# Optimization experiments

Measured on AMD Instinct MI355X. Metric: run time of the kernel, lower is better.

## Reference

```python
import jax, jax.numpy as jnp
import numpy as np

D = 128          # model_dim
R = 4            # num_relations
H = 64           # hidden width from num_neurons=[64, 64]
N = 50000        # num nodes
E = 800000       # num edges (avg degree 16)
NUM_NODE_TYPES = 3
UPDATE_NODE_TYPES = (0, 1)  # static update_node_type_indices
# update_edge_type_indices = range(R) (all relations), closed over statically


def setup_inputs() -> dict:
    key = jax.random.key(0)
    ks = jax.random.split(key, 12)
    s = 0.05
    return dict(
        node_feature=jax.random.normal(ks[0], (N, D), jnp.float32),
        src=jax.random.randint(ks[1], (E,), 0, N, dtype=jnp.int32),
        dst=jax.random.randint(ks[2], (E,), 0, N, dtype=jnp.int32),
        edge_type=jax.random.randint(ks[3], (E,), 0, R, dtype=jnp.int32),
        node_type=jax.random.randint(ks[4], (N,), 0, NUM_NODE_TYPES, dtype=jnp.int32),
        # per-relation MLP params, stacked over relations
        W1=jax.random.normal(ks[5], (R, D, H), jnp.float32) * s,
        b1=jnp.zeros((R, H), jnp.float32),
        W2=jax.random.normal(ks[6], (R, H, H), jnp.float32) * s,
        b2=jnp.zeros((R, H), jnp.float32),
        W3=jax.random.normal(ks[7], (R, H, D), jnp.float32) * s,
        b3=jnp.zeros((R, D), jnp.float32),
        # node updater: (R+1)*D -> H -> H -> D
        Wu1=jax.random.normal(ks[8], (D * (R + 1), H), jnp.float32) * s,
        bu1=jnp.zeros((H,), jnp.float32),
        Wu2=jax.random.normal(ks[9], (H, H), jnp.float32) * s,
        bu2=jnp.zeros((H,), jnp.float32),
        Wu3=jax.random.normal(ks[10], (H, D), jnp.float32) * s,
        bu3=jnp.zeros((D,), jnp.float32),
    )


def _mlp(x, W1, b1, W2, b2, W3, b3):
    # MLP with ReLU hidden layers, linear output (torch MLP(in, out, [64,64]))
    h = jax.nn.relu(x @ W1 + b1)
    h = jax.nn.relu(h @ W2 + b2)
    return h @ W3 + b3


def reference(node_feature, src, dst, edge_type, node_type,
              W1, b1, W2, b2, W3, b3, Wu1, bu1, Wu2, bu2, Wu3, bu3):
    n = node_feature.shape[0]
    sf = node_feature[src]  # [E, D] gather source features once

    # DGL send_and_recv only writes aggregated features to nodes that receive
    # at least one message; others are zero-filled. Track in-degree > 0.
    indeg = jax.ops.segment_sum(jnp.ones(dst.shape, node_feature.dtype), dst,
                                num_segments=n)
    has_in = (indeg > 0).astype(node_feature.dtype)[:, None]

    blocks = [jax.nn.relu(node_feature) * has_in]  # first D-block of enc input
    for i in range(W1.shape[0]):  # static loop over relations
        msg = jax.nn.relu(_mlp(sf, W1[i], b1[i], W2[i], b2[i], W3[i], b3[i]))
        msg = msg * (edge_type == i)[:, None]  # zero msg for other relations
        blocks.append(jax.ops.segment_sum(msg, dst, num_segments=n))
    enc = jnp.concatenate(blocks, axis=-1)  # [N, (R+1)*D]

    upd = _mlp(enc, Wu1, bu1, Wu2, bu2, Wu3, bu3)  # [N, D]
    upd_mask = jnp.zeros(node_type.shape, bool)
    for t in UPDATE_NODE_TYPES:
        upd_mask = upd_mask | (node_type == t)
    return jnp.where(upd_mask[:, None], upd, node_feature)
```

## Files before the change

### kernel.cpp

```cpp
#include <hip/hip_runtime.h>
#include <hip/hip_bf16.h>

#define D 128
#define H 64
#define R 4
#define NT 64
#define LDC 132
#define CAP 64
#define CCAP 4608
#define EPB 2048

typedef __attribute__((ext_vector_type(8))) short bf16x8;
typedef __attribute__((ext_vector_type(4))) float f32x4;

#define PREL 56
#define PFRAG 512
#define UBASE (R * PREL)
#define UPREL 40
#define NFRAG (UBASE + UPREL)

__device__ __forceinline__ float4 relu4(float4 v) {
    return make_float4(fmaxf(v.x, 0.f), fmaxf(v.y, 0.f), fmaxf(v.z, 0.f), fmaxf(v.w, 0.f));
}

__device__ __forceinline__ unsigned short f2bf_rne(float x) {
    unsigned u = __float_as_uint(x);
    return (unsigned short)((u + 0x7fffu + ((u >> 16) & 1u)) >> 16);
}

__device__ __forceinline__ void split1(float x, short& hi, short& lo) {
    unsigned u = __float_as_uint(x);
    unsigned hb = u & 0xffff0000u;
    float res = x - __uint_as_float(hb);
    hi = (short)(u >> 16);
    lo = (short)(__float_as_uint(res) >> 16);
}

__device__ __forceinline__ void split8(const float* x8, bf16x8& hi, bf16x8& lo) {
#pragma unroll
    for (int i = 0; i < 8; ++i) {
        short h, l;
        split1(x8[i], h, l);
        hi[i] = h; lo[i] = l;
    }
}

__device__ __forceinline__ void load_split_A(const float* ap, bf16x8& ah, bf16x8& al) {
    float x8[8];
    *(float4*)&x8[0] = *(const float4*)ap;
    *(float4*)&x8[4] = *(const float4*)(ap + 4);
    split8(x8, ah, al);
}

template<int KSTEPS>
__device__ __forceinline__ void split_strip_A(const float* Ws, int lane, bf16x8* ah, bf16x8* al) {
#pragma unroll
    for (int ks = 0; ks < KSTEPS; ++ks)
        load_split_A(Ws + (lane & 15) * LDC + ks * 32 + ((lane >> 4) << 3), ah[ks], al[ks]);
}

__device__ __forceinline__ void gload_lds16(const void* g, void* l) {
    __builtin_amdgcn_global_load_lds(
        (const __attribute__((address_space(1))) void*)g,
        (__attribute__((address_space(3))) void*)l, 16, 0, 0);
}

__device__ __forceinline__ void stage_chunk(const short* __restrict__ srcH,
                                            short* BbH, int w, int lane) {
#pragma unroll
    for (int f = w; f < 8; f += 4)
        gload_lds16(srcH + ((size_t)f << 9) + (lane << 3), BbH + (f << 9));
}

template<int NCH, int KSTEPS>
__device__ __forceinline__ void compute_chunk(const bf16x8* ah, const bf16x8* al,
                                              const short* BbH,
                                              const short* __restrict__ BloG,
                                              int lane, f32x4* acc) {
#pragma unroll
    for (int ks = 0; ks < KSTEPS; ++ks) {
        bf16x8 bh[NCH], bl[NCH];
#pragma unroll
        for (int n = 0; n < NCH; ++n) {
            int f = n * KSTEPS + ks;
            bh[n] = *(const bf16x8*)(BbH + ((f * 64 + lane) << 3));
            bl[n] = *(const bf16x8*)(BloG + (((size_t)f * 64 + lane) << 3));
        }
#pragma unroll
        for (int n = 0; n < NCH; ++n) {
            acc[n] = __builtin_amdgcn_mfma_f32_16x16x32_bf16(ah[ks], bh[n], acc[n], 0, 0, 0);
            acc[n] = __builtin_amdgcn_mfma_f32_16x16x32_bf16(ah[ks], bl[n], acc[n], 0, 0, 0);
            acc[n] = __builtin_amdgcn_mfma_f32_16x16x32_bf16(al[ks], bh[n], acc[n], 0, 0, 0);
        }
    }
}

template<int NT_TILES, int KSTEPS>
__device__ __forceinline__ void mfma_layer(const float* Als, int ld,
                                           const short* __restrict__ Bhi,
                                           const short* __restrict__ Blo,
                                           int lane, f32x4* acc) {
#pragma unroll
    for (int ks = 0; ks < KSTEPS; ++ks) {
        bf16x8 ah, al;
        load_split_A(Als + (lane & 15) * ld + ks * 32 + ((lane >> 4) << 3), ah, al);
        bf16x8 bh[NT_TILES], bl[NT_TILES];
#pragma unroll
        for (int n = 0; n < NT_TILES; ++n) {
            int f = n * KSTEPS + ks;
            bh[n] = *(const bf16x8*)(Bhi + (((size_t)f * 64 + lane) << 3));
            bl[n] = *(const bf16x8*)(Blo + (((size_t)f * 64 + lane) << 3));
        }
#pragma unroll
        for (int n = 0; n < NT_TILES; ++n) {
            acc[n] = __builtin_amdgcn_mfma_f32_16x16x32_bf16(ah, bh[n], acc[n], 0, 0, 0);
            acc[n] = __builtin_amdgcn_mfma_f32_16x16x32_bf16(ah, bl[n], acc[n], 0, 0, 0);
            acc[n] = __builtin_amdgcn_mfma_f32_16x16x32_bf16(al, bh[n], acc[n], 0, 0, 0);
        }
    }
}

template<int NT_TILES, int KSTEPS>
__device__ __forceinline__ void mfma_layer_regA(const bf16x8* ah, const bf16x8* al,
                                                const short* __restrict__ Bhi,
                                                const short* __restrict__ Blo,
                                                int lane, f32x4* acc) {
#pragma unroll
    for (int ks = 0; ks < KSTEPS; ++ks) {
        bf16x8 bh[NT_TILES], bl[NT_TILES];
#pragma unroll
        for (int n = 0; n < NT_TILES; ++n) {
            int f = n * KSTEPS + ks;
            bh[n] = *(const bf16x8*)(Bhi + (((size_t)f * 64 + lane) << 3));
            bl[n] = *(const bf16x8*)(Blo + (((size_t)f * 64 + lane) << 3));
        }
#pragma unroll
        for (int n = 0; n < NT_TILES; ++n) {
            acc[n] = __builtin_amdgcn_mfma_f32_16x16x32_bf16(ah[ks], bh[n], acc[n], 0, 0, 0);
            acc[n] = __builtin_amdgcn_mfma_f32_16x16x32_bf16(ah[ks], bl[n], acc[n], 0, 0, 0);
            acc[n] = __builtin_amdgcn_mfma_f32_16x16x32_bf16(al[ks], bh[n], acc[n], 0, 0, 0);
        }
    }
}

template<int NT_TILES>
__device__ __forceinline__ void store_C_lds(const f32x4* acc, const float* __restrict__ bias,
                                            float* Ld, int ld, int lane) {
    int r0 = (lane >> 4) << 2;
#pragma unroll
    for (int n = 0; n < NT_TILES; ++n) {
        int col = n * 16 + (lane & 15);
        float bv = bias[col];
#pragma unroll
        for (int q = 0; q < 4; ++q)
            Ld[(r0 + q) * ld + col] = fmaxf(acc[n][q] + bv, 0.f);
    }
}


__global__ __launch_bounds__(256) void k_prep(
    const float* __restrict__ W1, const float* __restrict__ W2,
    const float* __restrict__ W3, const float* __restrict__ Wu1,
    const float* __restrict__ Wu2, const float* __restrict__ Wu3,
    short* __restrict__ Phi, short* __restrict__ Plo,
    const int* __restrict__ esrc, const int* __restrict__ dst,
    const int* __restrict__ etype, int* __restrict__ gcnt,
    int2* __restrict__ coarse, int E, int NB)
{
    __shared__ int hist[256];
    __shared__ int base[256];
    const int t = threadIdx.x;

    if (blockIdx.x < 19) {
        int pair = blockIdx.x;
        const float* src; int KS, NTl, fragbase, ncol;
        if (pair < 16) {
            int r = pair >> 2, mat = pair & 3;
            if (mat == 0)      { src = W1  + (size_t)r * (D * H);       KS = 4; NTl = 4; fragbase = r * PREL + 0;  ncol = 64;  }
            else if (mat == 1) { src = W2  + (size_t)r * (H * H);       KS = 2; NTl = 4; fragbase = r * PREL + 16; ncol = 64;  }
            else if (mat == 2) { src = W3  + (size_t)r * (H * D);       KS = 2; NTl = 8; fragbase = r * PREL + 24; ncol = 128; }
            else               { src = Wu1 + (size_t)(r + 1) * D * H;   KS = 4; NTl = 4; fragbase = r * PREL + 40; ncol = 64;  }
        } else {
            int mat = pair - 16;
            if (mat == 0)      { src = Wu1; KS = 4; NTl = 4; fragbase = UBASE + 0;  ncol = 64;  }
            else if (mat == 1) { src = Wu2; KS = 2; NTl = 4; fragbase = UBASE + 16; ncol = 64;  }
            else               { src = Wu3; KS = 2; NTl = 8; fragbase = UBASE + 24; ncol = 128; }
        }
        int nf = NTl * KS;
        for (int u = t; u < nf * 64; u += 256) {
            int f = u >> 6, lane = u & 63;
            int n = f / KS, ks = f - n * KS;
            int col = n * 16 + (lane & 15);
            int k0 = ks * 32 + ((lane >> 4) << 3);
            size_t dstp = (((size_t)(fragbase + f)) * 64 + (size_t)lane) * 8;
#pragma unroll
            for (int i = 0; i < 8; ++i) {
                short h, l;
                split1(src[(size_t)(k0 + i) * ncol + col], h, l);
                Phi[dstp + i] = h;
                Plo[dstp + i] = l;
            }
        }
        return;
    }

    const int e0 = (blockIdx.x - 19) * EPB;
    hist[t] = 0;
    __syncthreads();
    int dsav[8], rsav[8];
#pragma unroll
    for (int j = 0; j < 8; ++j) {
        int e = e0 + j * 256 + t;
        int d = -1, rk = 0;
        if (e < E) {
            d = dst[e];
            rk = atomicAdd(&hist[d >> 8], 1);
        }
        dsav[j] = d; rsav[j] = rk;
    }
    __syncthreads();
    if (t < NB) base[t] = atomicAdd(&gcnt[t], hist[t]);
    __syncthreads();
#pragma unroll
    for (int j = 0; j < 8; ++j) {
        int e = e0 + j * 256 + t;
        int d = dsav[j];
        if (d >= 0) {
            int bin = d >> 8;
            int pos = base[bin] + rsav[j];
            if (pos < CCAP)
                coarse[(size_t)bin * CCAP + pos] = make_int2(d, esrc[e] * 4 + etype[e]);
        }
    }
}


__global__ __launch_bounds__(256, 3) void k_mlp_bin(
    const float* __restrict__ X,
    const float* __restrict__ b1, const float* __restrict__ b2, const float* __restrict__ b3,
    const short* __restrict__ Phi, const short* __restrict__ Plo,
    unsigned short* __restrict__ U, int N, int tiles,
    const int2* __restrict__ coarse, const int* __restrict__ gcnt,
    int* __restrict__ cnt, int* __restrict__ eidx, int NB)
{
    __shared__ float Bsh[NT * LDC];
    __shared__ short BbH[2][8 * PFRAG];

    const int tid = threadIdx.x;
    const int bid = blockIdx.x;

    if (bid < NB) {
        int* lcnt = (int*)Bsh;
        lcnt[tid] = 0;
        __syncthreads();
        int m = gcnt[bid]; if (m > CCAP) m = CCAP;
        const int2* cp = coarse + (size_t)bid * CCAP;
        for (int i = tid; i < m; i += 256) {
            int2 pr = cp[i];
            int p = atomicAdd(&lcnt[pr.x & 255], 1);
            if (p < CAP) eidx[(size_t)pr.x * CAP + p] = pr.y;
        }
        __syncthreads();
        int node = (bid << 8) + tid;
        if (node < N) cnt[node] = lcnt[tid];
        return;
    }

    const int mi = bid - NB;
    const int lane = tid & 63;
    const int w = tid >> 6;
    const int m16 = w * 16;
    const int r = mi / tiles;
    const int n0 = (mi - r * tiles) * NT;

    const short* PH = Phi + (size_t)(r * PREL) * PFRAG;
    const short* PL = Plo + (size_t)(r * PREL) * PFRAG;
    const float* b1r = b1 + r * H;
    const float* b2r = b2 + r * H;
    const float* b3r = b3 + r * D;

    float* Ws = &Bsh[m16 * LDC];

    stage_chunk(PH,             BbH[0], w, lane);
    stage_chunk(PH + 8 * PFRAG, BbH[1], w, lane);

    bf16x8 ahx[4], alx[4];
    {
        int row = n0 + m16 + (lane & 15);
        const float* xp = X + (size_t)row * D + ((lane >> 4) << 3);
        bool ok = (row < N);
#pragma unroll
        for (int ks = 0; ks < 4; ++ks) {
            float x8[8];
            if (ok) {
                *(float4*)&x8[0] = *(const float4*)(xp + ks * 32);
                *(float4*)&x8[4] = *(const float4*)(xp + ks * 32 + 4);
            } else {
#pragma unroll
                for (int i = 0; i < 8; ++i) x8[i] = 0.f;
            }
            split8(x8, ahx[ks], alx[ks]);
        }
    }
    __syncthreads();

    f32x4 acc[8];
#pragma unroll
    for (int n = 0; n < 4; ++n) acc[n] = (f32x4){0.f, 0.f, 0.f, 0.f};
    compute_chunk<2, 4>(ahx, alx, BbH[0], PL, lane, acc + 0);
    __syncthreads();
    stage_chunk(PH + 16 * PFRAG, BbH[0], w, lane);
    compute_chunk<2, 4>(ahx, alx, BbH[1], PL + 8 * PFRAG, lane, acc + 2);
    store_C_lds<4>(acc, b1r, Ws, LDC, lane);
    __syncthreads();
    stage_chunk(PH + 24 * PFRAG, BbH[1], w, lane);

    bf16x8 a2h[2], a2l[2];
    split_strip_A<2>(Ws, lane, a2h, a2l);
#pragma unroll
    for (int n = 0; n < 4; ++n) acc[n] = (f32x4){0.f, 0.f, 0.f, 0.f};
    compute_chunk<4, 2>(a2h, a2l, BbH[0], PL + 16 * PFRAG, lane, acc);
    store_C_lds<4>(acc, b2r, Ws, LDC, lane);
    __syncthreads();
    stage_chunk(PH + 32 * PFRAG, BbH[0], w, lane);

    bf16x8 a3h[2], a3l[2];
    split_strip_A<2>(Ws, lane, a3h, a3l);
#pragma unroll
    for (int n = 0; n < 8; ++n) acc[n] = (f32x4){0.f, 0.f, 0.f, 0.f};
    compute_chunk<4, 2>(a3h, a3l, BbH[1], PL + 24 * PFRAG, lane, acc + 0);
    __syncthreads();
    stage_chunk(PH + 40 * PFRAG, BbH[1], w, lane);
    compute_chunk<4, 2>(a3h, a3l, BbH[0], PL + 32 * PFRAG, lane, acc + 4);
    store_C_lds<8>(acc, b3r, Ws, LDC, lane);
    __syncthreads();
    stage_chunk(PH + 48 * PFRAG, BbH[0], w, lane);

    bf16x8 auh[4], aul[4];
    split_strip_A<4>(Ws, lane, auh, aul);
    f32x4 accu[4];
#pragma unroll
    for (int n = 0; n < 4; ++n) accu[n] = (f32x4){0.f, 0.f, 0.f, 0.f};
    compute_chunk<2, 4>(auh, aul, BbH[1], PL + 40 * PFRAG, lane, accu + 0);
    __syncthreads();
    compute_chunk<2, 4>(auh, aul, BbH[0], PL + 48 * PFRAG, lane, accu + 2);
    {
        int r0 = (lane >> 4) << 2;
#pragma unroll
        for (int n = 0; n < 4; ++n) {
            int col = n * 16 + (lane & 15);
#pragma unroll
            for (int q = 0; q < 4; ++q) {
                int node = n0 + m16 + r0 + q;
                if (node < N)
                    U[((size_t)node * R + r) * H + col] = f2bf_rne(accu[n][q]);
            }
        }
    }
}


__global__ __launch_bounds__(256) void k_gather(
    const unsigned int* __restrict__ U32,
    const int* __restrict__ cnt, const int* __restrict__ eidx,
    float* __restrict__ S, int N)
{
    const int wid = threadIdx.x >> 6, lane = threadIdx.x & 63;
    const int n = blockIdx.x * 4 + wid;
    if (n >= N) return;
    int g = cnt[n]; if (g > CAP) g = CAP;
    const int* ep = eidx + (size_t)n * CAP;
    const int half = lane >> 5;
    const int c2 = lane & 31;
    float ax = 0.f, ay = 0.f;
    {
        int m = g;
        int v = 0;
        if (lane < m) v = ep[lane];
        for (int j0 = 0; j0 < m; j0 += 16) {
            int lim = m - j0; if (lim > 16) lim = 16;
            unsigned t[8];
#pragma unroll
            for (int p = 0; p < 8; ++p) {
                int vi = __shfl(v, j0 + 2 * p + half);
                bool ok = (2 * p + half) < lim;
                t[p] = ok ? U32[(size_t)vi * 32 + c2] : 0u;
            }
#pragma unroll
            for (int p = 0; p < 8; ++p) {
                ax += __uint_as_float(t[p] << 16);
                ay += __uint_as_float(t[p] & 0xffff0000u);
            }
        }
    }
    ax += __shfl_xor(ax, 32);
    ay += __shfl_xor(ay, 32);
    if (half == 0)
        *(float2*)&S[(size_t)n * H + (c2 << 1)] = make_float2(ax, ay);
}


__global__ __launch_bounds__(256, 4) void k_upd(
    const float* __restrict__ X, const float* __restrict__ S,
    const int* __restrict__ cnt, const int* __restrict__ node_type,
    const short* __restrict__ Phi, const short* __restrict__ Plo,
    const float* __restrict__ bu1, const float* __restrict__ bu2, const float* __restrict__ bu3,
    float* __restrict__ out, int N)
{
    __shared__ float Hsh[NT * LDC];

    const int tid = threadIdx.x;
    const int lane = tid & 63;
    const int w = tid >> 6;
    const int m16 = w * 16;
    const int n0 = blockIdx.x * NT;

    const short* PH = Phi + (size_t)UBASE * PFRAG;
    const short* PL = Plo + (size_t)UBASE * PFRAG;

    float* Ws = &Hsh[m16 * LDC];

    bf16x8 ahx[4], alx[4];
    {
        int row = n0 + m16 + (lane & 15);
        bool ok = (row < N) && (cnt[row] > 0);
        const float* xp = X + (size_t)row * D + ((lane >> 4) << 3);
#pragma unroll
        for (int ks = 0; ks < 4; ++ks) {
            float x8[8];
            if (ok) {
                float4 a = *(const float4*)(xp + ks * 32);
                float4 b = *(const float4*)(xp + ks * 32 + 4);
                a = relu4(a); b = relu4(b);
                *(float4*)&x8[0] = a;
                *(float4*)&x8[4] = b;
            } else {
#pragma unroll
                for (int i = 0; i < 8; ++i) x8[i] = 0.f;
            }
            split8(x8, ahx[ks], alx[ks]);
        }
    }

    f32x4 acc[8];
#pragma unroll
    for (int n = 0; n < 4; ++n) acc[n] = (f32x4){0.f, 0.f, 0.f, 0.f};
    mfma_layer_regA<4, 4>(ahx, alx, PH, PL, lane, acc);
    {
        int r0 = (lane >> 4) << 2;
#pragma unroll
        for (int n = 0; n < 4; ++n) {
            int col = n * 16 + (lane & 15);
            float bv = bu1[col];
#pragma unroll
            for (int q = 0; q < 4; ++q) {
                int node = n0 + m16 + r0 + q;
                float sv = (node < N) ? S[(size_t)node * H + col] : 0.f;
                Ws[(r0 + q) * LDC + col] = fmaxf(acc[n][q] + bv + sv, 0.f);
            }
        }
    }

#pragma unroll
    for (int n = 0; n < 4; ++n) acc[n] = (f32x4){0.f, 0.f, 0.f, 0.f};
    mfma_layer<4, 2>(Ws, LDC, PH + (size_t)16 * PFRAG, PL + (size_t)16 * PFRAG, lane, acc);
    store_C_lds<4>(acc, bu2, Ws, LDC, lane);

#pragma unroll
    for (int n = 0; n < 8; ++n) acc[n] = (f32x4){0.f, 0.f, 0.f, 0.f};
    mfma_layer<8, 2>(Ws, LDC, PH + (size_t)24 * PFRAG, PL + (size_t)24 * PFRAG, lane, acc);
    {
        int r0 = (lane >> 4) << 2;
#pragma unroll
        for (int q = 0; q < 4; ++q) {
            int node = n0 + m16 + r0 + q;
            if (node >= N) continue;
            int t = node_type[node];
#pragma unroll
            for (int n = 0; n < 8; ++n) {
                int col = n * 16 + (lane & 15);
                float o = (t <= 1) ? (acc[n][q] + bu3[col])
                                   : X[(size_t)node * D + col];
                out[(size_t)node * D + col] = o;
            }
        }
    }
}

extern "C" void kernel_launch(void* const* d_in, const int* in_sizes, int n_in,
                              void* d_out, int out_size, void* d_ws, size_t ws_size,
                              hipStream_t stream) {
    const float* X     = (const float*)d_in[0];
    const int*   src   = (const int*)d_in[1];
    const int*   dst   = (const int*)d_in[2];
    const int*   etype = (const int*)d_in[3];
    const int*   ntype = (const int*)d_in[4];
    const float* W1    = (const float*)d_in[5];
    const float* b1    = (const float*)d_in[6];
    const float* W2    = (const float*)d_in[7];
    const float* b2    = (const float*)d_in[8];
    const float* W3    = (const float*)d_in[9];
    const float* b3    = (const float*)d_in[10];
    const float* Wu1   = (const float*)d_in[11];
    const float* bu1   = (const float*)d_in[12];
    const float* Wu2   = (const float*)d_in[13];
    const float* bu2   = (const float*)d_in[14];
    const float* Wu3   = (const float*)d_in[15];
    const float* bu3   = (const float*)d_in[16];
    float* out = (float*)d_out;

    const int N = in_sizes[4];
    const int E = in_sizes[1];
    const int NB = (N + 255) >> 8;

    unsigned short* U = (unsigned short*)d_ws;
    float* S    = (float*)(U + (size_t)N * R * H);
    int* cnt    = (int*)(S + (size_t)N * H);
    int* gcnt   = cnt + N;
    int* eidx   = gcnt + 256;
    int2* coarse = (int2*)(eidx + (size_t)N * CAP);
    short* Phi  = (short*)(coarse + (size_t)NB * CCAP);
    short* Plo  = Phi + (size_t)NFRAG * PFRAG;

    hipMemsetAsync(gcnt, 0, 256 * sizeof(int), stream);

    int binAB = (E + EPB - 1) / EPB;
    k_prep<<<19 + binAB, 256, 0, stream>>>(W1, W2, W3, Wu1, Wu2, Wu3, Phi, Plo,
                                           src, dst, etype, gcnt, coarse, E, NB);

    int tiles = (N + NT - 1) / NT;
    k_mlp_bin<<<NB + tiles * R, 256, 0, stream>>>(X, b1, b2, b3, Phi, Plo, U, N, tiles,
                                                  coarse, gcnt, cnt, eidx, NB);
    k_gather<<<(N + 3) / 4, 256, 0, stream>>>((const unsigned int*)U, cnt, eidx, S, N);
    k_upd<<<tiles, 256, 0, stream>>>(X, S, cnt, ntype, Phi, Plo, bu1, bu2, bu3, out, N);
}
```

Baseline: 132.5 us.

## Stage update-MLP hi weight fragments through double-buffered LDS in k_upd

The node-update kernel now copies the high-half bf16 weight fragments into a two-slot shared-memory buffer in chunks and computes from LDS, while the low halves still come from global memory. This reuses the edge kernel's compute_chunk and stage_chunk helpers and drops the separate global-load layer functions. The aim is to cut repeated global weight traffic per wave and overlap staging of the next chunk with compute. In exchange it adds shared memory use and several block-wide barriers, and lowers the occupancy hint from 4 to 3 blocks per CU.

```diff
diff --git a/kernel.cpp b/kernel.cpp
--- a/kernel.cpp
+++ b/kernel.cpp
@@ -88,54 +88,6 @@
         }
 #pragma unroll
         for (int n = 0; n < NCH; ++n) {
-            acc[n] = __builtin_amdgcn_mfma_f32_16x16x32_bf16(ah[ks], bh[n], acc[n], 0, 0, 0);
-            acc[n] = __builtin_amdgcn_mfma_f32_16x16x32_bf16(ah[ks], bl[n], acc[n], 0, 0, 0);
-            acc[n] = __builtin_amdgcn_mfma_f32_16x16x32_bf16(al[ks], bh[n], acc[n], 0, 0, 0);
-        }
-    }
-}
-
-template<int NT_TILES, int KSTEPS>
-__device__ __forceinline__ void mfma_layer(const float* Als, int ld,
-                                           const short* __restrict__ Bhi,
-                                           const short* __restrict__ Blo,
-                                           int lane, f32x4* acc) {
-#pragma unroll
-    for (int ks = 0; ks < KSTEPS; ++ks) {
-        bf16x8 ah, al;
-        load_split_A(Als + (lane & 15) * ld + ks * 32 + ((lane >> 4) << 3), ah, al);
-        bf16x8 bh[NT_TILES], bl[NT_TILES];
-#pragma unroll
-        for (int n = 0; n < NT_TILES; ++n) {
-            int f = n * KSTEPS + ks;
-            bh[n] = *(const bf16x8*)(Bhi + (((size_t)f * 64 + lane) << 3));
-            bl[n] = *(const bf16x8*)(Blo + (((size_t)f * 64 + lane) << 3));
-        }
-#pragma unroll
-        for (int n = 0; n < NT_TILES; ++n) {
-            acc[n] = __builtin_amdgcn_mfma_f32_16x16x32_bf16(ah, bh[n], acc[n], 0, 0, 0);
-            acc[n] = __builtin_amdgcn_mfma_f32_16x16x32_bf16(ah, bl[n], acc[n], 0, 0, 0);
-            acc[n] = __builtin_amdgcn_mfma_f32_16x16x32_bf16(al, bh[n], acc[n], 0, 0, 0);
-        }
-    }
-}
-
-template<int NT_TILES, int KSTEPS>
-__device__ __forceinline__ void mfma_layer_regA(const bf16x8* ah, const bf16x8* al,
-                                                const short* __restrict__ Bhi,
-                                                const short* __restrict__ Blo,
-                                                int lane, f32x4* acc) {
-#pragma unroll
-    for (int ks = 0; ks < KSTEPS; ++ks) {
-        bf16x8 bh[NT_TILES], bl[NT_TILES];
-#pragma unroll
-        for (int n = 0; n < NT_TILES; ++n) {
-            int f = n * KSTEPS + ks;
-            bh[n] = *(const bf16x8*)(Bhi + (((size_t)f * 64 + lane) << 3));
-            bl[n] = *(const bf16x8*)(Blo + (((size_t)f * 64 + lane) << 3));
-        }
-#pragma unroll
-        for (int n = 0; n < NT_TILES; ++n) {
             acc[n] = __builtin_amdgcn_mfma_f32_16x16x32_bf16(ah[ks], bh[n], acc[n], 0, 0, 0);
             acc[n] = __builtin_amdgcn_mfma_f32_16x16x32_bf16(ah[ks], bl[n], acc[n], 0, 0, 0);
             acc[n] = __builtin_amdgcn_mfma_f32_16x16x32_bf16(al[ks], bh[n], acc[n], 0, 0, 0);
@@ -400,7 +352,7 @@
 }
 
 
-__global__ __launch_bounds__(256, 4) void k_upd(
+__global__ __launch_bounds__(256, 3) void k_upd(
     const float* __restrict__ X, const float* __restrict__ S,
     const int* __restrict__ cnt, const int* __restrict__ node_type,
     const short* __restrict__ Phi, const short* __restrict__ Plo,
@@ -408,6 +360,7 @@
     float* __restrict__ out, int N)
 {
     __shared__ float Hsh[NT * LDC];
+    __shared__ short UbH[2][8 * PFRAG];
 
     const int tid = threadIdx.x;
     const int lane = tid & 63;
@@ -419,6 +372,9 @@
     const short* PL = Plo + (size_t)UBASE * PFRAG;
 
     float* Ws = &Hsh[m16 * LDC];
+
+    stage_chunk(PH,             UbH[0], w, lane);
+    stage_chunk(PH + 8 * PFRAG, UbH[1], w, lane);
 
     bf16x8 ahx[4], alx[4];
     {
@@ -441,11 +397,15 @@
             split8(x8, ahx[ks], alx[ks]);
         }
     }
+    __syncthreads();
 
     f32x4 acc[8];
 #pragma unroll
     for (int n = 0; n < 4; ++n) acc[n] = (f32x4){0.f, 0.f, 0.f, 0.f};
-    mfma_layer_regA<4, 4>(ahx, alx, PH, PL, lane, acc);
+    compute_chunk<2, 4>(ahx, alx, UbH[0], PL, lane, acc + 0);
+    __syncthreads();
+    stage_chunk(PH + 16 * PFRAG, UbH[0], w, lane);
+    compute_chunk<2, 4>(ahx, alx, UbH[1], PL + 8 * PFRAG, lane, acc + 2);
     {
         int r0 = (lane >> 4) << 2;
 #pragma unroll
@@ -460,15 +420,25 @@
             }
         }
     }
-
+    __syncthreads();
+    stage_chunk(PH + 24 * PFRAG, UbH[1], w, lane);
+
+    bf16x8 a2h[2], a2l[2];
+    split_strip_A<2>(Ws, lane, a2h, a2l);
 #pragma unroll
     for (int n = 0; n < 4; ++n) acc[n] = (f32x4){0.f, 0.f, 0.f, 0.f};
-    mfma_layer<4, 2>(Ws, LDC, PH + (size_t)16 * PFRAG, PL + (size_t)16 * PFRAG, lane, acc);
+    compute_chunk<4, 2>(a2h, a2l, UbH[0], PL + 16 * PFRAG, lane, acc);
     store_C_lds<4>(acc, bu2, Ws, LDC, lane);
-
+    __syncthreads();
+    stage_chunk(PH + 32 * PFRAG, UbH[0], w, lane);
+
+    bf16x8 a3h[2], a3l[2];
+    split_strip_A<2>(Ws, lane, a3h, a3l);
 #pragma unroll
     for (int n = 0; n < 8; ++n) acc[n] = (f32x4){0.f, 0.f, 0.f, 0.f};
-    mfma_layer<8, 2>(Ws, LDC, PH + (size_t)24 * PFRAG, PL + (size_t)24 * PFRAG, lane, acc);
+    compute_chunk<4, 2>(a3h, a3l, UbH[1], PL + 24 * PFRAG, lane, acc + 0);
+    __syncthreads();
+    compute_chunk<4, 2>(a3h, a3l, UbH[0], PL + 32 * PFRAG, lane, acc + 4);
     {
         int r0 = (lane >> 4) << 2;
 #pragma unroll
```

Result: slower. 141.8 us (+7.0%).
